# Performance work log

Measured on AMD Instinct MI355X. Metric: run time of the kernel, lower is better.

Reference implementation:

```python
import jax, jax.numpy as jnp
import numpy as np

DFAUD = 1024
DFRGB = 1024
DIM_K = 1024
N_HEADS = 4
B, T = 16, 1024


def setup_inputs() -> dict:
    key = jax.random.key(0)
    ks = jax.random.split(key, 11)
    s = lambda d: 1.0 / np.sqrt(d)
    return {
        "x": jax.random.normal(ks[0], (B, T, DFAUD), jnp.float32),
        "y": jax.random.normal(ks[1], (B, T, DFRGB), jnp.float32),
        "adj": jax.random.normal(ks[2], (B, T, T), jnp.float32),
        "Wq": jax.random.uniform(ks[3], (DIM_K, DFAUD), jnp.float32, -s(DFAUD), s(DFAUD)),
        "bq": jnp.zeros((DIM_K,), jnp.float32),
        "Wk": jax.random.uniform(ks[4], (DIM_K, DFRGB), jnp.float32, -s(DFRGB), s(DFRGB)),
        "bk": jnp.zeros((DIM_K,), jnp.float32),
        "Wv": jax.random.uniform(ks[5], (DIM_K, DFRGB), jnp.float32, -s(DFRGB), s(DFRGB)),
        "bv": jnp.zeros((DIM_K,), jnp.float32),
        "Wo": jax.random.uniform(ks[6], (DFRGB, DIM_K), jnp.float32, -s(DIM_K), s(DIM_K)),
        "bo": jnp.zeros((DFRGB,), jnp.float32),
    }


def reference(x, y, adj, Wq, bq, Wk, bk, Wv, bv, Wo, bo):
    b, t = x.shape[0], x.shape[1]
    dh = DIM_K // N_HEADS
    norm = 1.0 / np.sqrt(DIM_K)
    # Faithful reproduction of the torch reshape(-1, B, T, dim_k // n_heads):
    # [B, T, dim_k] -> [n_heads, B, T, dh] (row-major reshape, layout-mixing for h>1)
    Q = (x @ Wq.T + bq).reshape(N_HEADS, b, t, dh)
    K = (y @ Wk.T + bk).reshape(N_HEADS, b, t, dh)
    V = (y @ Wv.T + bv).reshape(N_HEADS, b, t, dh)
    scores = jnp.einsum('hbqd,hbkd->hbqk', Q, K) * norm  # [h, B, T, T]
    att = jax.nn.softmax(scores + adj, axis=-1)          # adj [B,T,T] broadcasts
    temp = jnp.einsum('hbqk,hbkd->hbqd', att, V).reshape(b, t, DIM_K)
    out = (temp @ Wo.T + bo).reshape(-1, t, y.shape[2])
    return out
```

## Files before the change

### kernel.cpp

```cpp
#include <hip/hip_runtime.h>
#include <stdint.h>

typedef unsigned short u16;
typedef __attribute__((ext_vector_type(8))) short short8_t;
typedef __attribute__((ext_vector_type(4))) float f32x4;

typedef const __attribute__((address_space(1))) void GV;
typedef __attribute__((address_space(3))) void LV;

__device__ __forceinline__ void gload_lds16(const void* g, void* l) {
  __builtin_amdgcn_global_load_lds((GV*)g, (LV*)l, 16, 0, 0);
}

__device__ __forceinline__ u16 f2bf(float f) {
  union { float f; uint32_t u; } v; v.f = f;
  return (u16)((v.u + 0x7FFFu + ((v.u >> 16) & 1u)) >> 16);
}

__device__ __forceinline__ f32x4 fz4() { f32x4 v = {0.f, 0.f, 0.f, 0.f}; return v; }

__global__ __launch_bounds__(256) void cast_kernel(const float* __restrict__ in,
                                                   u16* __restrict__ out) {
  int i = (blockIdx.x * 256 + threadIdx.x) * 4;
  float4 v = *(const float4*)(in + i);
  ushort4 o;
  o.x = f2bf(v.x); o.y = f2bf(v.y); o.z = f2bf(v.z); o.w = f2bf(v.w);
  *(ushort4*)(out + i) = o;
}

template <int OUT_BF16>
__global__ __launch_bounds__(512, 2) void gemm8(const u16* __restrict__ A,
                                                const u16* __restrict__ B,
                                                const float* __restrict__ bias,
                                                void* __restrict__ Cout,
                                                int M, int N, int K) {
  __shared__ u16 Al[2 * 16384];
  __shared__ u16 Bl[2 * 16384];
  const int tid = threadIdx.x, w = tid >> 6, l = tid & 63;
  const int g = l >> 4, q = l & 15;
  const int n0 = blockIdx.x * 256, m0 = blockIdx.y * 256;
  const int wr = (w >> 2) * 128, wc = (w & 3) * 64;
  const int NT = K >> 6;
  const int ah = w >> 2;
  const int bh = (w & 3) >> 1;
  const int brow0 = ((w & 3) & 1) * 64;

#define STAGE_A(S, half)                                                          \
  {                                                                               \
    _Pragma("unroll") for (int j_ = 0; j_ < 2; ++j_) {                            \
      const int idx_ = j_ * 512 + tid;                                            \
      const int row_ = idx_ >> 3;                                                 \
      const int sl_ = (idx_ & 7) ^ (((idx_ >> 5) & 1) << 1);                      \
      gload_lds16(A + (size_t)(m0 + (half) * 128 + row_) * K + (S) * 64 + sl_ * 8,\
                  Al + ((S) & 1) * 16384 + (half) * 8192 + (j_ * 512 + w * 64) * 8);\
    }                                                                             \
  }
#define STAGE_B(S, half)                                                          \
  {                                                                               \
    _Pragma("unroll") for (int j_ = 0; j_ < 2; ++j_) {                            \
      const int idx_ = j_ * 512 + tid;                                            \
      const int row_ = idx_ >> 3;                                                 \
      const int sl_ = (idx_ & 7) ^ (((idx_ >> 5) & 1) << 1);                      \
      gload_lds16(B + (size_t)(n0 + (half) * 128 + row_) * K + (S) * 64 + sl_ * 8,\
                  Bl + ((S) & 1) * 16384 + (half) * 8192 + (j_ * 512 + w * 64) * 8);\
    }                                                                             \
  }

  f32x4 acc[8][4];
#pragma unroll
  for (int i = 0; i < 8; ++i)
#pragma unroll
    for (int n = 0; n < 4; ++n) acc[i][n] = fz4();

  float bv[4];
#pragma unroll
  for (int nf = 0; nf < 4; ++nf) bv[nf] = bias[n0 + wc + nf * 16 + q];

  STAGE_A(0, 0); STAGE_A(0, 1); STAGE_B(0, 0); STAGE_B(0, 1);
  STAGE_A(1, 0); STAGE_A(1, 1); STAGE_B(1, 0); STAGE_B(1, 1);
  asm volatile("s_waitcnt vmcnt(8)");
  __builtin_amdgcn_s_barrier();

  short8_t bfr[4][2];
  for (int S = 0; S < NT; ++S) {
    const int bs = (S & 1) * 16384;
#pragma unroll
    for (int p = 0; p < 4; ++p) {
      short8_t afr[2][2];
#pragma unroll
      for (int mi = 0; mi < 2; ++mi)
#pragma unroll
        for (int kk = 0; kk < 2; ++kk) {
          const int r = (2 * p + mi) * 16 + q;
          afr[mi][kk] = *(const short8_t*)(Al + bs + ah * 8192 + r * 64 +
                                           ((kk * 4 + g) ^ (((r >> 2) & 1) << 1)) * 8);
        }
      if (p == 0) {
#pragma unroll
        for (int nf = 0; nf < 4; ++nf)
#pragma unroll
          for (int kk = 0; kk < 2; ++kk) {
            const int r = brow0 + nf * 16 + q;
            bfr[nf][kk] = *(const short8_t*)(Bl + bs + bh * 8192 + r * 64 +
                                             ((kk * 4 + g) ^ (((r >> 2) & 1) << 1)) * 8);
          }
      }
      if (p == 0 && S >= 1 && S + 1 < NT) STAGE_A(S + 1, 0);
      if (p == 1 && S >= 1 && S + 1 < NT) STAGE_A(S + 1, 1);
      if (p == 2 && S + 2 < NT) STAGE_B(S + 2, 0);
      if (p == 3 && S + 2 < NT) STAGE_B(S + 2, 1);
      if (p == 3) {
        if (S == NT - 2) { asm volatile("s_waitcnt vmcnt(0)"); }
        else if (S < NT - 2) { asm volatile("s_waitcnt vmcnt(4)"); }
      }
      __builtin_amdgcn_s_barrier();
      asm volatile("s_waitcnt lgkmcnt(0)" ::: "memory");
      __builtin_amdgcn_sched_barrier(0);
      __builtin_amdgcn_s_setprio(1);
#pragma unroll
      for (int nf = 0; nf < 4; ++nf)
#pragma unroll
        for (int mi = 0; mi < 2; ++mi)
#pragma unroll
          for (int kk = 0; kk < 2; ++kk)
            acc[2 * p + mi][nf] = __builtin_amdgcn_mfma_f32_16x16x32_bf16(
                afr[mi][kk], bfr[nf][kk], acc[2 * p + mi][nf], 0, 0, 0);
      __builtin_amdgcn_s_setprio(0);
      __builtin_amdgcn_s_barrier();
    }
  }
#undef STAGE_A
#undef STAGE_B

#pragma unroll
  for (int nf = 0; nf < 4; ++nf) {
    const int col = n0 + wc + nf * 16 + q;
#pragma unroll
    for (int mf = 0; mf < 8; ++mf) {
      const int rowb = m0 + wr + mf * 16 + g * 4;
#pragma unroll
      for (int j = 0; j < 4; ++j) {
        const float vv = acc[mf][nf][j] + bv[nf];
        if (OUT_BF16)
          ((u16*)Cout)[(size_t)(rowb + j) * N + col] = f2bf(vv);
        else
          ((float*)Cout)[(size_t)(rowb + j) * N + col] = vv;
      }
    }
  }
}

__global__ __launch_bounds__(256) void transpose_v(const u16* __restrict__ V,
                                                   u16* __restrict__ VT) {
  __shared__ u16 t[64][68];
  const int hb = blockIdx.z;
  const int t0 = blockIdx.x * 64, d0 = blockIdx.y * 64;
  const u16* src = V + (size_t)hb * 1024 * 256;
  u16* dst = VT + (size_t)hb * 256 * 1024;
  const int tid = threadIdx.x;
#pragma unroll
  for (int i = 0; i < 4; ++i) {
    const int idx = i * 256 + tid;
    const int r = idx >> 4, c4 = (idx & 15) * 4;
    ushort4 v = *(const ushort4*)(src + (size_t)(t0 + r) * 256 + d0 + c4);
    *(ushort4*)&t[r][c4] = v;
  }
  __syncthreads();
#pragma unroll
  for (int i = 0; i < 4; ++i) {
    const int idx = i * 256 + tid;
    const int r = idx >> 4, c4 = (idx & 15) * 4;
    ushort4 v;
    v.x = t[c4][r]; v.y = t[c4 + 1][r]; v.z = t[c4 + 2][r]; v.w = t[c4 + 3][r];
    *(ushort4*)(dst + (size_t)(d0 + r) * 1024 + t0 + c4) = v;
  }
}

__global__ __launch_bounds__(256, 2) void attn_kernel(const u16* __restrict__ Q,
                                                      const u16* __restrict__ Kf,
                                                      const u16* __restrict__ VT,
                                                      const float* __restrict__ adj,
                                                      u16* __restrict__ O) {
  __shared__ u16 Ks[2][32 * 256];
  __shared__ u16 Vs[2][256 * 32];
  __shared__ u16 Ps[4][16 * 32];
  const int tid = threadIdx.x, w = tid >> 6, l = tid & 63;
  const int g = l >> 4, q = l & 15;
  const int bid = blockIdx.x;
  const int xcd = bid & 7, idx = bid >> 3;
  const int b = xcd * 2 + (idx >> 6);
  const int qb = (idx >> 2) & 15, h = idx & 3;
  const int hb = h * 16 + b;
  const int q0 = qb * 64;
  const u16* qb_p = Q + ((size_t)hb * 1024 + q0 + w * 16) * 256;
  const u16* kb = Kf + (size_t)hb * 1024 * 256;
  const u16* vtb = VT + (size_t)hb * 256 * 1024;
  const float* adjr = adj + (size_t)b * 1024 * 1024 + (size_t)(q0 + w * 16 + q) * 1024;

  short8_t qf[8];
#pragma unroll
  for (int kk = 0; kk < 8; ++kk)
    qf[kk] = *(const short8_t*)(qb_p + (size_t)q * 256 + kk * 32 + g * 8);

  f32x4 o[16];
#pragma unroll
  for (int n = 0; n < 16; ++n) o[n] = fz4();
  float mrun = -1e30f, lrun = 0.f;

#define STAGE_KV(ktt, bufi)                                                        \
  {                                                                                \
    _Pragma("unroll") for (int i_ = 0; i_ < 4; ++i_) {                             \
      const int c_ = w * 4 + i_;                                                   \
      const int row_ = 2 * c_ + (l >> 5);                                          \
      const int gcb_ = ((l & 31) ^ (row_ & 7)) * 16;                               \
      gload_lds16((const char*)(kb + (size_t)((ktt) * 32 + row_) * 256) + gcb_,    \
                  (char*)Ks[bufi] + c_ * 1024);                                    \
    }                                                                              \
    _Pragma("unroll") for (int i_ = 0; i_ < 4; ++i_) {                             \
      const int c_ = w * 4 + i_;                                                   \
      const int dr_ = c_ * 16 + (l >> 2);                                          \
      const int sl_ = (l & 3) ^ ((dr_ >> 1) & 3);                                  \
      gload_lds16((const char*)(vtb + (size_t)dr_ * 1024 + (ktt) * 32) + sl_ * 16, \
                  (char*)Vs[bufi] + c_ * 1024);                                    \
    }                                                                              \
  }

  STAGE_KV(0, 0);
  float4 a0 = *(const float4*)(adjr + 0 * 32 + 0 * 16 + g * 4);
  float4 a1 = *(const float4*)(adjr + 0 * 32 + 1 * 16 + g * 4);
  __syncthreads();

  for (int kt = 0; kt < 32; ++kt) {
    const int cur = kt & 1;
    float4 n0v = a0, n1v = a1;
    if (kt < 31) {
      STAGE_KV(kt + 1, cur ^ 1);
      n0v = *(const float4*)(adjr + (kt + 1) * 32 + 0 * 16 + g * 4);
      n1v = *(const float4*)(adjr + (kt + 1) * 32 + 1 * 16 + g * 4);
    }

    f32x4 s[2];
    const char* kbuf = (const char*)Ks[cur];
    __builtin_amdgcn_s_setprio(1);
#pragma unroll
    for (int f = 0; f < 2; ++f) {
      f32x4 a = fz4();
      const int row = f * 16 + q;
      const char* kr = kbuf + row * 512;
#pragma unroll
      for (int kk = 0; kk < 8; ++kk) {
        const int cb = kk * 64 + g * 16;
        short8_t kfr = *(const short8_t*)(kr + (cb ^ ((row & 7) << 4)));
        a = __builtin_amdgcn_mfma_f32_16x16x32_bf16(kfr, qf[kk], a, 0, 0, 0);
      }
      s[f] = a;
    }
    __builtin_amdgcn_s_setprio(0);

#pragma unroll
    for (int j = 0; j < 4; ++j) {
      s[0][j] = s[0][j] * 0.03125f + ((const float*)&a0)[j];
      s[1][j] = s[1][j] * 0.03125f + ((const float*)&a1)[j];
    }

    float pmax = s[0][0];
#pragma unroll
    for (int j = 1; j < 4; ++j) pmax = fmaxf(pmax, s[0][j]);
#pragma unroll
    for (int j = 0; j < 4; ++j) pmax = fmaxf(pmax, s[1][j]);
    pmax = fmaxf(pmax, __shfl_xor(pmax, 16));
    pmax = fmaxf(pmax, __shfl_xor(pmax, 32));

    if (!__all(pmax - mrun <= 8.0f)) {
      const float mn = fmaxf(mrun, pmax);
      const float al = __expf(mrun - mn);
      mrun = mn;
      lrun *= al;
#pragma unroll
      for (int n = 0; n < 16; ++n)
#pragma unroll
        for (int r = 0; r < 4; ++r) o[n][r] *= al;
    }

    float sum = 0.f;
#pragma unroll
    for (int f = 0; f < 2; ++f)
#pragma unroll
      for (int j = 0; j < 4; ++j) {
        const float p = __expf(s[f][j] - mrun);
        s[f][j] = p;
        sum += p;
      }
    sum += __shfl_xor(sum, 16);
    sum += __shfl_xor(sum, 32);
    lrun += sum;

    {
      char* pw = (char*)Ps[w] + q * 64;
      const int swz = (q >> 1) & 3;
#pragma unroll
      for (int f = 0; f < 2; ++f) {
        ushort4 pk;
        pk.x = f2bf(s[f][0]); pk.y = f2bf(s[f][1]);
        pk.z = f2bf(s[f][2]); pk.w = f2bf(s[f][3]);
        *(ushort4*)(pw + ((f * 32 + g * 8) ^ (swz << 4))) = pk;
      }
    }
    asm volatile("s_waitcnt lgkmcnt(0)");
    __builtin_amdgcn_sched_barrier(0);
    short8_t pa = *(const short8_t*)((const char*)Ps[w] + q * 64 +
                                     ((g * 16) ^ (((q >> 1) & 3) << 4)));

    const char* vbuf = (const char*)Vs[cur];
    __builtin_amdgcn_s_setprio(1);
#pragma unroll
    for (int n = 0; n < 16; ++n) {
      const int dr = n * 16 + q;
      const int sl = g ^ ((dr >> 1) & 3);
      short8_t vf = *(const short8_t*)(vbuf + dr * 64 + sl * 16);
      o[n] = __builtin_amdgcn_mfma_f32_16x16x32_bf16(vf, pa, o[n], 0, 0, 0);
    }
    __builtin_amdgcn_s_setprio(0);

    __syncthreads();
    a0 = n0v; a1 = n1v;
  }
#undef STAGE_KV

  const float inv = 1.0f / lrun;
  u16* ob = O + ((size_t)hb * 1024 + q0 + w * 16 + q) * 256;
#pragma unroll
  for (int n = 0; n < 16; ++n) {
    ushort4 st;
    st.x = f2bf(o[n][0] * inv); st.y = f2bf(o[n][1] * inv);
    st.z = f2bf(o[n][2] * inv); st.w = f2bf(o[n][3] * inv);
    *(ushort4*)(ob + n * 16 + g * 4) = st;
  }
}

extern "C" void kernel_launch(void* const* d_in, const int* in_sizes, int n_in,
                              void* d_out, int out_size, void* d_ws, size_t ws_size,
                              hipStream_t stream) {
  (void)in_sizes; (void)n_in; (void)out_size; (void)ws_size;
  const float* x   = (const float*)d_in[0];
  const float* y   = (const float*)d_in[1];
  const float* adj = (const float*)d_in[2];
  const float* Wq  = (const float*)d_in[3];
  const float* bq  = (const float*)d_in[4];
  const float* Wk  = (const float*)d_in[5];
  const float* bk  = (const float*)d_in[6];
  const float* Wv  = (const float*)d_in[7];
  const float* bv  = (const float*)d_in[8];
  const float* Wo  = (const float*)d_in[9];
  const float* bo  = (const float*)d_in[10];

  char* ws = (char*)d_ws;
  const size_t MB = 1ull << 20;
  u16* Xb  = (u16*)(ws + 0);
  u16* Yb  = (u16*)(ws + 32 * MB);
  u16* Wqb = (u16*)(ws + 64 * MB);
  u16* Wkb = (u16*)(ws + 66 * MB);
  u16* Wvb = (u16*)(ws + 68 * MB);
  u16* Wob = (u16*)(ws + 70 * MB);
  u16* Qb  = (u16*)(ws + 72 * MB);
  u16* Kb  = (u16*)(ws + 104 * MB);
  u16* Vb  = (u16*)(ws + 136 * MB);
  u16* VTb = (u16*)(ws + 168 * MB);
  u16* Tmp = Xb;

  cast_kernel<<<16384, 256, 0, stream>>>(x, Xb);
  cast_kernel<<<16384, 256, 0, stream>>>(y, Yb);
  cast_kernel<<<1024, 256, 0, stream>>>(Wq, Wqb);
  cast_kernel<<<1024, 256, 0, stream>>>(Wk, Wkb);
  cast_kernel<<<1024, 256, 0, stream>>>(Wv, Wvb);
  cast_kernel<<<1024, 256, 0, stream>>>(Wo, Wob);

  dim3 gg(4, 64);
  gemm8<1><<<gg, 512, 0, stream>>>(Xb, Wqb, bq, Qb, 16384, 1024, 1024);
  gemm8<1><<<gg, 512, 0, stream>>>(Yb, Wkb, bk, Kb, 16384, 1024, 1024);
  gemm8<1><<<gg, 512, 0, stream>>>(Yb, Wvb, bv, Vb, 16384, 1024, 1024);

  transpose_v<<<dim3(16, 4, 64), 256, 0, stream>>>(Vb, VTb);

  attn_kernel<<<1024, 256, 0, stream>>>(Qb, Kb, VTb, adj, Tmp);

  gemm8<0><<<gg, 512, 0, stream>>>(Tmp, Wob, bo, d_out, 16384, 1024, 1024);
}
```

Before: 383.7 us.

## Single-buffer K/V LDS with register staging to raise attention occupancy

Replaces the double-buffered direct global-to-LDS K/V staging with a single LDS buffer, prefetching the next tile into registers and writing it to LDS between two barriers. Launch bounds go from 2 to 4 blocks per CU, which halves LDS per block and aims to let more waves hide memory latency. In exchange it adds a second barrier per iteration, costs 8 extra short8 registers per thread for staging, and may cause spills under the tighter register cap.

```diff
diff --git a/kernel.cpp b/kernel.cpp
--- a/kernel.cpp
+++ b/kernel.cpp
@@ -176,13 +176,13 @@
   }
 }
 
-__global__ __launch_bounds__(256, 2) void attn_kernel(const u16* __restrict__ Q,
+__global__ __launch_bounds__(256, 4) void attn_kernel(const u16* __restrict__ Q,
                                                       const u16* __restrict__ Kf,
                                                       const u16* __restrict__ VT,
                                                       const float* __restrict__ adj,
                                                       u16* __restrict__ O) {
-  __shared__ u16 Ks[2][32 * 256];
-  __shared__ u16 Vs[2][256 * 32];
+  __shared__ u16 Ks[32 * 256];
+  __shared__ u16 Vs[256 * 32];
   __shared__ u16 Ps[4][16 * 32];
   const int tid = threadIdx.x, w = tid >> 6, l = tid & 63;
   const int g = l >> 4, q = l & 15;
@@ -197,6 +197,11 @@
   const u16* vtb = VT + (size_t)hb * 256 * 1024;
   const float* adjr = adj + (size_t)b * 1024 * 1024 + (size_t)(q0 + w * 16 + q) * 1024;
 
+  const int krow_b = tid >> 5;
+  const int kslot = tid & 31;
+  const int vdr_b = tid >> 2;
+  const int vsl = tid & 3;
+
   short8_t qf[8];
 #pragma unroll
   for (int kk = 0; kk < 8; ++kk)
@@ -207,46 +212,54 @@
   for (int n = 0; n < 16; ++n) o[n] = fz4();
   float mrun = -1e30f, lrun = 0.f;
 
-#define STAGE_KV(ktt, bufi)                                                        \
+  short8_t kst[4], vst[4];
+
+#define LOADREGS(ktt)                                                              \
   {                                                                                \
     _Pragma("unroll") for (int i_ = 0; i_ < 4; ++i_) {                             \
-      const int c_ = w * 4 + i_;                                                   \
-      const int row_ = 2 * c_ + (l >> 5);                                          \
-      const int gcb_ = ((l & 31) ^ (row_ & 7)) * 16;                               \
-      gload_lds16((const char*)(kb + (size_t)((ktt) * 32 + row_) * 256) + gcb_,    \
-                  (char*)Ks[bufi] + c_ * 1024);                                    \
+      const int row_ = i_ * 8 + krow_b;                                            \
+      kst[i_] = *(const short8_t*)(kb + (size_t)((ktt) * 32 + row_) * 256 +        \
+                                   kslot * 8);                                     \
     }                                                                              \
     _Pragma("unroll") for (int i_ = 0; i_ < 4; ++i_) {                             \
-      const int c_ = w * 4 + i_;                                                   \
-      const int dr_ = c_ * 16 + (l >> 2);                                          \
-      const int sl_ = (l & 3) ^ ((dr_ >> 1) & 3);                                  \
-      gload_lds16((const char*)(vtb + (size_t)dr_ * 1024 + (ktt) * 32) + sl_ * 16, \
-                  (char*)Vs[bufi] + c_ * 1024);                                    \
+      const int dr_ = i_ * 64 + vdr_b;                                             \
+      vst[i_] = *(const short8_t*)(vtb + (size_t)dr_ * 1024 + (ktt) * 32 +         \
+                                   vsl * 8);                                       \
     }                                                                              \
   }
-
-  STAGE_KV(0, 0);
+#define WRITEREGS()                                                                \
+  {                                                                                \
+    _Pragma("unroll") for (int i_ = 0; i_ < 4; ++i_) {                             \
+      const int row_ = i_ * 8 + krow_b;                                            \
+      *(short8_t*)((char*)Ks + row_ * 512 + ((kslot ^ (row_ & 7)) * 16)) = kst[i_];\
+    }                                                                              \
+    _Pragma("unroll") for (int i_ = 0; i_ < 4; ++i_) {                             \
+      const int dr_ = i_ * 64 + vdr_b;                                             \
+      *(short8_t*)((char*)Vs + dr_ * 64 + ((vsl ^ ((dr_ >> 1) & 3)) * 16)) = vst[i_];\
+    }                                                                              \
+  }
+
+  LOADREGS(0);
   float4 a0 = *(const float4*)(adjr + 0 * 32 + 0 * 16 + g * 4);
   float4 a1 = *(const float4*)(adjr + 0 * 32 + 1 * 16 + g * 4);
+  WRITEREGS();
   __syncthreads();
 
   for (int kt = 0; kt < 32; ++kt) {
-    const int cur = kt & 1;
     float4 n0v = a0, n1v = a1;
     if (kt < 31) {
-      STAGE_KV(kt + 1, cur ^ 1);
+      LOADREGS(kt + 1);
       n0v = *(const float4*)(adjr + (kt + 1) * 32 + 0 * 16 + g * 4);
       n1v = *(const float4*)(adjr + (kt + 1) * 32 + 1 * 16 + g * 4);
     }
 
     f32x4 s[2];
-    const char* kbuf = (const char*)Ks[cur];
     __builtin_amdgcn_s_setprio(1);
 #pragma unroll
     for (int f = 0; f < 2; ++f) {
       f32x4 a = fz4();
       const int row = f * 16 + q;
-      const char* kr = kbuf + row * 512;
+      const char* kr = (const char*)Ks + row * 512;
 #pragma unroll
       for (int kk = 0; kk < 8; ++kk) {
         const int cb = kk * 64 + g * 16;
@@ -311,21 +324,25 @@
     short8_t pa = *(const short8_t*)((const char*)Ps[w] + q * 64 +
                                      ((g * 16) ^ (((q >> 1) & 3) << 4)));
 
-    const char* vbuf = (const char*)Vs[cur];
     __builtin_amdgcn_s_setprio(1);
 #pragma unroll
     for (int n = 0; n < 16; ++n) {
       const int dr = n * 16 + q;
       const int sl = g ^ ((dr >> 1) & 3);
-      short8_t vf = *(const short8_t*)(vbuf + dr * 64 + sl * 16);
+      short8_t vf = *(const short8_t*)((const char*)Vs + dr * 64 + sl * 16);
       o[n] = __builtin_amdgcn_mfma_f32_16x16x32_bf16(vf, pa, o[n], 0, 0, 0);
     }
     __builtin_amdgcn_s_setprio(0);
 
-    __syncthreads();
+    if (kt < 31) {
+      __syncthreads();
+      WRITEREGS();
+      __syncthreads();
+    }
     a0 = n0v; a1 = n1v;
   }
-#undef STAGE_KV
+#undef LOADREGS
+#undef WRITEREGS
 
   const float inv = 1.0f / lrun;
   u16* ob = O + ((size_t)hb * 1024 + q0 + w * 16 + q) * 256;
```

Result: slower. 585.4 us (+52.6%).
